# Performance work log

Hardware: AMD Instinct MI355X
Metric: run time of the kernel (lower is better)

The kernel has to match this reference:

```python
import jax, jax.numpy as jnp
import numpy as np

N_NODES = 50000
N_EDGES = 800000
IN_C, HID_C, OUT_C = 512, 256, 128


def setup_inputs() -> dict:
    key = jax.random.key(0)
    k1, k2, k3, k4, k5, k6 = jax.random.split(key, 6)
    x = jax.random.normal(k1, (N_NODES, IN_C), dtype=jnp.float32)
    edge_index = jax.random.randint(k2, (2, N_EDGES), 0, N_NODES, dtype=jnp.int64)
    # Glorot-ish init for linear weights, zero bias (PyG GCNConv default)
    W1 = jax.random.normal(k3, (IN_C, HID_C), dtype=jnp.float32) / np.sqrt(IN_C)
    b1 = jnp.zeros((HID_C,), dtype=jnp.float32)
    W2 = jax.random.normal(k4, (HID_C, OUT_C), dtype=jnp.float32) / np.sqrt(HID_C)
    b2 = jnp.zeros((OUT_C,), dtype=jnp.float32)
    return {"x": x, "edge_index": edge_index, "W1": W1, "b1": b1, "W2": W2, "b2": b2}


def _gcn_layer(h, src, dst, norm, W, b, n_nodes):
    # h: [N, Fin] -> [N, Fout];  out_i = sum_{j->i} norm_e * (h W)_j + b
    h = h @ W
    msg = h[src] * norm[:, None]            # [E+N, Fout]
    out = jax.ops.segment_sum(msg, dst, num_segments=n_nodes)
    return out + b


def reference(x, edge_index, W1, b1, W2, b2):
    n = x.shape[0]
    loops = jnp.arange(n, dtype=edge_index.dtype)
    src = jnp.concatenate([edge_index[0], loops])  # add self-loops
    dst = jnp.concatenate([edge_index[1], loops])
    # symmetric normalization D^{-1/2} (A+I) D^{-1/2}
    deg = jax.ops.segment_sum(jnp.ones_like(src, dtype=x.dtype), dst, num_segments=n)
    dinv = jax.lax.rsqrt(jnp.maximum(deg, 1.0))
    norm = dinv[src] * dinv[dst]

    h = _gcn_layer(x, src, dst, norm, W1, b1, n)
    h = jax.nn.relu(h)
    # dropout: identity in eval mode (training=False)
    out = _gcn_layer(h, src, dst, norm, W2, b2, n)
    return out
```

## Files before the change

kernel.cpp:

```cpp
#include <hip/hip_runtime.h>
#include <hip/hip_bf16.h>

#define N_NODES 50000
#define N_EDGES 800000
#define IN_C 512
#define HID_C 256
#define OUT_C 128
#define SCAN_BLOCKS 49

typedef short bf16x8 __attribute__((ext_vector_type(8)));
typedef float f32x4 __attribute__((ext_vector_type(4)));
typedef float f32x2 __attribute__((ext_vector_type(2)));

__device__ __forceinline__ float bf2f(unsigned short u) {
    return __uint_as_float(((unsigned)u) << 16);
}
__device__ __forceinline__ unsigned short f2bf(float f) {
    __hip_bfloat16 h = __float2bfloat16(f);
    return *(unsigned short*)&h;
}
__device__ __forceinline__ void acc_fp8x4(int dw, float* a) {
    f32x2 lo = __builtin_amdgcn_cvt_pk_f32_fp8(dw, false);
    f32x2 hi = __builtin_amdgcn_cvt_pk_f32_fp8(dw, true);
    a[0] += lo[0]; a[1] += lo[1]; a[2] += hi[0]; a[3] += hi[1];
}
__device__ __forceinline__ unsigned char f2fp8(float f) {
    return (unsigned char)(__builtin_amdgcn_cvt_pk_fp8_f32(f, 0.0f, 0, false) & 0xff);
}

__global__ void zero_counts_kernel(int* __restrict__ counts) {
    int i = blockIdx.x * blockDim.x + threadIdx.x;
    if (i < N_NODES) counts[i] = 0;
}

__global__ void count_kernel(const int* __restrict__ ei, int* __restrict__ counts) {
    int e = blockIdx.x * blockDim.x + threadIdx.x;
    if (e < N_EDGES) atomicAdd(&counts[ei[N_EDGES + e]], 1);
}

__global__ __launch_bounds__(256) void scan_part_kernel(const int* __restrict__ counts,
                                                        int* __restrict__ excl,
                                                        int* __restrict__ bsums) {
    __shared__ int tsum[256];
    const int t = threadIdx.x;
    const int base = blockIdx.x * 1024 + t * 4;
    int v[4];
    int s = 0;
#pragma unroll
    for (int j = 0; j < 4; j++) {
        int idx = base + j;
        v[j] = (idx < N_NODES) ? counts[idx] : 0;
        s += v[j];
    }
    tsum[t] = s;
    __syncthreads();
    for (int off = 1; off < 256; off <<= 1) {
        int add = (t >= off) ? tsum[t - off] : 0;
        __syncthreads();
        tsum[t] += add;
        __syncthreads();
    }
    int run = tsum[t] - s;
#pragma unroll
    for (int j = 0; j < 4; j++) {
        int idx = base + j;
        if (idx < N_NODES) excl[idx] = run;
        run += v[j];
    }
    if (t == 255) bsums[blockIdx.x] = tsum[255];
}

__global__ void scan_sums_kernel(int* __restrict__ bsums) {
    int ln = threadIdx.x;
    int v = (ln < SCAN_BLOCKS) ? bsums[ln] : 0;
    for (int off = 1; off < 64; off <<= 1) {
        int u = __shfl_up(v, off, 64);
        if (ln >= off) v += u;
    }
    int excl = __shfl_up(v, 1, 64);
    if (ln == 0) excl = 0;
    if (ln < SCAN_BLOCKS) bsums[ln] = excl;
}

__global__ void add_dinv_kernel(int* __restrict__ offsets, const int* __restrict__ bsums,
                                int* __restrict__ woff, const int* __restrict__ counts,
                                float* __restrict__ dinv) {
    int i = blockIdx.x * blockDim.x + threadIdx.x;
    if (i < N_NODES) {
        int o = offsets[i] + bsums[i >> 10];
        offsets[i] = o;
        woff[i] = o;
        dinv[i] = rsqrtf(1.0f + (float)counts[i]);
    }
    if (i == 0) offsets[N_NODES] = N_EDGES;
}

__global__ void fill_kernel(const int* __restrict__ ei, int* __restrict__ woff,
                            int* __restrict__ sedge) {
    int e = blockIdx.x * blockDim.x + threadIdx.x;
    if (e < N_EDGES) {
        int s = ei[e];
        int d = ei[N_EDGES + e];
        int pos = atomicAdd(&woff[d], 1);
        sedge[pos] = s;
    }
}

__global__ __launch_bounds__(256) void tcast_kernel(const float* __restrict__ W,
                                                    unsigned short* __restrict__ WT,
                                                    int K, int N) {
    int idx = blockIdx.x * 256 + threadIdx.x;
    int n = idx / K, k = idx - n * K;
    WT[idx] = f2bf(W[(size_t)k * N + n]);
}

__global__ __launch_bounds__(256) void gemm1_fused(const float* __restrict__ x,
                                                   const unsigned short* __restrict__ BT,
                                                   unsigned char* __restrict__ C,
                                                   const float* __restrict__ dinv) {
    __shared__ unsigned short As[64 * 32];
    __shared__ unsigned short Bs[256 * 32];

    const int tid = threadIdx.x;
    const int w = tid >> 6;
    const int ln = tid & 63;
    const int br = blockIdx.x * 64;

    const int quad = ln >> 4;
    const int l16 = ln & 15;
    const int wc = w * 64;

    const int ar = tid >> 2;
    const int ak = (tid & 3) * 8;

    int arow = br + ar;
    arow = arow < N_NODES ? arow : N_NODES - 1;
    const float* xrow = x + (size_t)arow * IN_C + ak;

    f32x4 acc[4][4];
#pragma unroll
    for (int mt = 0; mt < 4; mt++)
#pragma unroll
        for (int nt = 0; nt < 4; nt++) acc[mt][nt] = (f32x4){0.f, 0.f, 0.f, 0.f};

    for (int kk = 0; kk < IN_C; kk += 32) {
        float4 v0 = *(const float4*)(xrow + kk);
        float4 v1 = *(const float4*)(xrow + kk + 4);
        bf16x8 a8;
        a8[0] = (short)f2bf(v0.x); a8[1] = (short)f2bf(v0.y);
        a8[2] = (short)f2bf(v0.z); a8[3] = (short)f2bf(v0.w);
        a8[4] = (short)f2bf(v1.x); a8[5] = (short)f2bf(v1.y);
        a8[6] = (short)f2bf(v1.z); a8[7] = (short)f2bf(v1.w);
        *(bf16x8*)&As[ar * 32 + ak] = a8;
#pragma unroll
        for (int t = 0; t < 4; t++) {
            int n = (tid >> 2) + 64 * t;
            const unsigned short* gp = BT + (size_t)n * IN_C + kk + ak;
            unsigned short* lp = Bs + t * 2048 + tid * 8;
            __builtin_amdgcn_global_load_lds((const __attribute__((address_space(1))) void*)gp,
                                             (__attribute__((address_space(3))) void*)lp,
                                             16, 0, 0);
        }
        __syncthreads();

        bf16x8 af[4], bfr[4];
#pragma unroll
        for (int mt = 0; mt < 4; mt++)
            af[mt] = *(const bf16x8*)&As[(mt * 16 + l16) * 32 + quad * 8];
#pragma unroll
        for (int nt = 0; nt < 4; nt++)
            bfr[nt] = *(const bf16x8*)&Bs[(wc + nt * 16 + l16) * 32 + quad * 8];
#pragma unroll
        for (int mt = 0; mt < 4; mt++)
#pragma unroll
            for (int nt = 0; nt < 4; nt++)
                acc[mt][nt] = __builtin_amdgcn_mfma_f32_16x16x32_bf16(af[mt], bfr[nt],
                                                                      acc[mt][nt], 0, 0, 0);
        __syncthreads();
    }

#pragma unroll
    for (int mt = 0; mt < 4; mt++) {
#pragma unroll
        for (int r = 0; r < 4; r++) {
            int gr = br + mt * 16 + quad * 4 + r;
            if (gr < N_NODES) {
                float ds = dinv[gr];
#pragma unroll
                for (int nt = 0; nt < 4; nt++) {
                    int gc = wc + nt * 16 + l16;
                    C[(size_t)gr * HID_C + gc] = f2fp8(ds * acc[mt][nt][r]);
                }
            }
        }
    }
}

__global__ __launch_bounds__(256) void mfma_gemm_bt(const unsigned short* __restrict__ A,
                                                    const unsigned short* __restrict__ BT,
                                                    unsigned short* __restrict__ C,
                                                    const float* __restrict__ dinv,
                                                    int M, int N, int K) {
    __shared__ unsigned short As[128 * 32];
    __shared__ unsigned short Bs[128 * 32];

    const int tid = threadIdx.x;
    const int w = tid >> 6;
    const int ln = tid & 63;
    const int br = blockIdx.y * 128;
    const int bc = blockIdx.x * 128;

    const int quad = ln >> 4;
    const int l16 = ln & 15;
    const int wr = (w >> 1) * 64;
    const int wc = (w & 1) * 64;

    const int crow = ln >> 2;
    const int koff = (ln & 3) * 8;

    f32x4 acc[4][4];
#pragma unroll
    for (int mt = 0; mt < 4; mt++)
#pragma unroll
        for (int nt = 0; nt < 4; nt++) acc[mt][nt] = (f32x4){0.f, 0.f, 0.f, 0.f};

    for (int kk = 0; kk < K; kk += 32) {
#pragma unroll
        for (int t = 0; t < 2; t++) {
            int c = w + t * 4;
            int row = br + c * 16 + crow;
            row = row < M ? row : M - 1;
            const unsigned short* gp = A + (size_t)row * K + kk + koff;
            unsigned short* lp = As + c * 512 + ln * 8;
            __builtin_amdgcn_global_load_lds((const __attribute__((address_space(1))) void*)gp,
                                             (__attribute__((address_space(3))) void*)lp,
                                             16, 0, 0);
        }
#pragma unroll
        for (int t = 0; t < 2; t++) {
            int c = w + t * 4;
            int row = bc + c * 16 + crow;
            const unsigned short* gp = BT + (size_t)row * K + kk + koff;
            unsigned short* lp = Bs + c * 512 + ln * 8;
            __builtin_amdgcn_global_load_lds((const __attribute__((address_space(1))) void*)gp,
                                             (__attribute__((address_space(3))) void*)lp,
                                             16, 0, 0);
        }
        __syncthreads();

        bf16x8 af[4], bfr[4];
#pragma unroll
        for (int mt = 0; mt < 4; mt++)
            af[mt] = *(const bf16x8*)&As[(wr + mt * 16 + l16) * 32 + quad * 8];
#pragma unroll
        for (int nt = 0; nt < 4; nt++)
            bfr[nt] = *(const bf16x8*)&Bs[(wc + nt * 16 + l16) * 32 + quad * 8];
#pragma unroll
        for (int mt = 0; mt < 4; mt++)
#pragma unroll
            for (int nt = 0; nt < 4; nt++)
                acc[mt][nt] = __builtin_amdgcn_mfma_f32_16x16x32_bf16(af[mt], bfr[nt],
                                                                      acc[mt][nt], 0, 0, 0);
        __syncthreads();
    }

#pragma unroll
    for (int mt = 0; mt < 4; mt++) {
#pragma unroll
        for (int r = 0; r < 4; r++) {
            int gr = br + wr + mt * 16 + quad * 4 + r;
            if (gr < M) {
                float ds = dinv[gr];
#pragma unroll
                for (int nt = 0; nt < 4; nt++) {
                    int gc = bc + wc + nt * 16 + l16;
                    C[(size_t)gr * N + gc] = f2bf(ds * acc[mt][nt][r]);
                }
            }
        }
    }
}

__global__ __launch_bounds__(256) void gather1_fp8(const int* __restrict__ offsets,
                                                   const int* __restrict__ sedge,
                                                   const unsigned char* __restrict__ H,
                                                   const float* __restrict__ dinv,
                                                   const float* __restrict__ bias,
                                                   unsigned short* __restrict__ out) {
    const int node = blockIdx.x * 4 + (threadIdx.x >> 6);
    if (node >= N_NODES) return;
    const int ln = threadIdx.x & 63;
    const int g = ln >> 5;
    const int l = ln & 31;
    const int c0 = l * 8;

    float acc[8] = {};
    if (g == 0) {
        uint2 d = *(const uint2*)&H[(size_t)node * HID_C + c0];
        acc_fp8x4((int)d.x, acc);
        acc_fp8x4((int)d.y, acc + 4);
    }

    int k = offsets[node] + g;
    const int k1 = offsets[node + 1];
    for (; k + 6 < k1; k += 8) {
        int s0 = sedge[k], s1 = sedge[k + 2], s2 = sedge[k + 4], s3 = sedge[k + 6];
        uint2 d0 = *(const uint2*)&H[(size_t)s0 * HID_C + c0];
        uint2 d1 = *(const uint2*)&H[(size_t)s1 * HID_C + c0];
        uint2 d2 = *(const uint2*)&H[(size_t)s2 * HID_C + c0];
        uint2 d3 = *(const uint2*)&H[(size_t)s3 * HID_C + c0];
        acc_fp8x4((int)d0.x, acc); acc_fp8x4((int)d0.y, acc + 4);
        acc_fp8x4((int)d1.x, acc); acc_fp8x4((int)d1.y, acc + 4);
        acc_fp8x4((int)d2.x, acc); acc_fp8x4((int)d2.y, acc + 4);
        acc_fp8x4((int)d3.x, acc); acc_fp8x4((int)d3.y, acc + 4);
    }
    for (; k < k1; k += 2) {
        int s0 = sedge[k];
        uint2 d0 = *(const uint2*)&H[(size_t)s0 * HID_C + c0];
        acc_fp8x4((int)d0.x, acc);
        acc_fp8x4((int)d0.y, acc + 4);
    }

#pragma unroll
    for (int j = 0; j < 8; j++) acc[j] += __shfl_xor(acc[j], 32, 64);

    if (g == 0) {
        const float di = dinv[node];
        bf16x8 o;
#pragma unroll
        for (int j = 0; j < 8; j++)
            o[j] = (short)f2bf(fmaxf(di * acc[j] + bias[c0 + j], 0.0f));
        *(bf16x8*)&out[(size_t)node * HID_C + c0] = o;
    }
}

__global__ __launch_bounds__(256) void gather2_bf16(const int* __restrict__ offsets,
                                                    const int* __restrict__ sedge,
                                                    const unsigned short* __restrict__ H,
                                                    const float* __restrict__ dinv,
                                                    const float* __restrict__ bias,
                                                    float* __restrict__ out) {
    const int node = blockIdx.x * 4 + (threadIdx.x >> 6);
    if (node >= N_NODES) return;
    const int ln = threadIdx.x & 63;
    const int g = ln >> 4;
    const int l = ln & 15;
    const int c0 = l * 8;

    float acc[8] = {};
    if (g == 0) {
        bf16x8 h = *(const bf16x8*)&H[(size_t)node * OUT_C + c0];
#pragma unroll
        for (int j = 0; j < 8; j++) acc[j] = bf2f((unsigned short)h[j]);
    }

    int k = offsets[node] + g;
    const int k1 = offsets[node + 1];
    for (; k + 12 < k1; k += 16) {
        int s0 = sedge[k], s1 = sedge[k + 4], s2 = sedge[k + 8], s3 = sedge[k + 12];
        bf16x8 h0 = *(const bf16x8*)&H[(size_t)s0 * OUT_C + c0];
        bf16x8 h1 = *(const bf16x8*)&H[(size_t)s1 * OUT_C + c0];
        bf16x8 h2 = *(const bf16x8*)&H[(size_t)s2 * OUT_C + c0];
        bf16x8 h3 = *(const bf16x8*)&H[(size_t)s3 * OUT_C + c0];
#pragma unroll
        for (int j = 0; j < 8; j++) {
            acc[j] += bf2f((unsigned short)h0[j]);
            acc[j] += bf2f((unsigned short)h1[j]);
            acc[j] += bf2f((unsigned short)h2[j]);
            acc[j] += bf2f((unsigned short)h3[j]);
        }
    }
    for (; k < k1; k += 4) {
        int s0 = sedge[k];
        bf16x8 h0 = *(const bf16x8*)&H[(size_t)s0 * OUT_C + c0];
#pragma unroll
        for (int j = 0; j < 8; j++) acc[j] += bf2f((unsigned short)h0[j]);
    }

#pragma unroll
    for (int m = 16; m < 64; m <<= 1) {
#pragma unroll
        for (int j = 0; j < 8; j++) acc[j] += __shfl_xor(acc[j], m, 64);
    }

    if (g == 0) {
        const float di = dinv[node];
        float o[8];
#pragma unroll
        for (int j = 0; j < 8; j++) o[j] = di * acc[j] + bias[c0 + j];
        *(float4*)&out[(size_t)node * OUT_C + c0] = make_float4(o[0], o[1], o[2], o[3]);
        *(float4*)&out[(size_t)node * OUT_C + c0 + 4] = make_float4(o[4], o[5], o[6], o[7]);
    }
}

extern "C" void kernel_launch(void* const* d_in, const int* in_sizes, int n_in,
                              void* d_out, int out_size, void* d_ws, size_t ws_size,
                              hipStream_t stream) {
    const float* x  = (const float*)d_in[0];
    const int*   ei = (const int*)d_in[1];
    const float* W1 = (const float*)d_in[2];
    const float* b1 = (const float*)d_in[3];
    const float* W2 = (const float*)d_in[4];
    const float* b2 = (const float*)d_in[5];
    float* out = (float*)d_out;

    int*   counts     = (int*)d_ws;
    int*   offsets    = counts + 50048;
    int*   woff       = offsets + 50052;
    int*   bsums      = woff + 50048;
    float* dinv       = (float*)(bsums + 64);
    int*   sedge      = (int*)(dinv + 50048);
    unsigned short* W1T = (unsigned short*)(sedge + 800000);
    unsigned short* W2T = W1T + 131072;
    unsigned short* xb  = W2T + 32768;
    unsigned char*  H1  = (unsigned char*)(xb + (size_t)N_NODES * IN_C);
    unsigned short* A1b = xb;
    unsigned short* H2  = xb + (size_t)N_NODES * HID_C;

    zero_counts_kernel<<<(N_NODES + 255) / 256, 256, 0, stream>>>(counts);
    count_kernel<<<(N_EDGES + 255) / 256, 256, 0, stream>>>(ei, counts);
    scan_part_kernel<<<SCAN_BLOCKS, 256, 0, stream>>>(counts, offsets, bsums);
    scan_sums_kernel<<<1, 64, 0, stream>>>(bsums);
    add_dinv_kernel<<<(N_NODES + 255) / 256, 256, 0, stream>>>(offsets, bsums, woff, counts, dinv);
    fill_kernel<<<(N_EDGES + 255) / 256, 256, 0, stream>>>(ei, woff, sedge);

    tcast_kernel<<<(IN_C * HID_C) / 256, 256, 0, stream>>>(W1, W1T, IN_C, HID_C);
    tcast_kernel<<<(HID_C * OUT_C) / 256, 256, 0, stream>>>(W2, W2T, HID_C, OUT_C);

    gemm1_fused<<<(N_NODES + 63) / 64, 256, 0, stream>>>(x, W1T, H1, dinv);
    gather1_fp8<<<(N_NODES + 3) / 4, 256, 0, stream>>>(offsets, sedge, H1, dinv, b1, A1b);

    {
        dim3 grid(OUT_C / 128, (N_NODES + 127) / 128);
        mfma_gemm_bt<<<grid, 256, 0, stream>>>(A1b, W2T, H2, dinv, N_NODES, OUT_C, HID_C);
    }
    gather2_bf16<<<(N_NODES + 3) / 4, 256, 0, stream>>>(offsets, sedge, H2, dinv, b2, out);
}
```

Baseline: 386.2 us.

## Double-buffer LDS tiles in both GEMMs and shrink GEMM2 row tile

Both GEMM kernels now use two LDS buffers, so the global loads for the next K slice are issued before the MFMAs on the current slice and one barrier per iteration is removed. GEMM1 also delays the fp32-to-bf16 conversion of the next A tile until after the MFMAs. GEMM2 is specialised to fixed sizes with 64-row blocks instead of 128, which launches more blocks over the 50k rows. The cost is doubled LDS per block and more live registers, which may lower occupancy.

```diff
diff --git a/kernel.cpp b/kernel.cpp
--- a/kernel.cpp
+++ b/kernel.cpp
@@ -26,6 +26,10 @@
 }
 __device__ __forceinline__ unsigned char f2fp8(float f) {
     return (unsigned char)(__builtin_amdgcn_cvt_pk_fp8_f32(f, 0.0f, 0, false) & 0xff);
+}
+__device__ __forceinline__ void glds16(const void* gp, void* lp) {
+    __builtin_amdgcn_global_load_lds((const __attribute__((address_space(1))) void*)gp,
+                                     (__attribute__((address_space(3))) void*)lp, 16, 0, 0);
 }
 
 __global__ void zero_counts_kernel(int* __restrict__ counts) {
@@ -118,8 +122,8 @@
                                                    const unsigned short* __restrict__ BT,
                                                    unsigned char* __restrict__ C,
                                                    const float* __restrict__ dinv) {
-    __shared__ unsigned short As[64 * 32];
-    __shared__ unsigned short Bs[256 * 32];
+    __shared__ unsigned short As[2][64 * 32];
+    __shared__ unsigned short Bs[2][256 * 32];
 
     const int tid = threadIdx.x;
     const int w = tid >> 6;
@@ -136,6 +140,7 @@
     int arow = br + ar;
     arow = arow < N_NODES ? arow : N_NODES - 1;
     const float* xrow = x + (size_t)arow * IN_C + ak;
+    const int brow = (tid >> 2);
 
     f32x4 acc[4][4];
 #pragma unroll
@@ -143,39 +148,60 @@
 #pragma unroll
         for (int nt = 0; nt < 4; nt++) acc[mt][nt] = (f32x4){0.f, 0.f, 0.f, 0.f};
 
-    for (int kk = 0; kk < IN_C; kk += 32) {
-        float4 v0 = *(const float4*)(xrow + kk);
-        float4 v1 = *(const float4*)(xrow + kk + 4);
+    {
+        float4 v0 = *(const float4*)(xrow);
+        float4 v1 = *(const float4*)(xrow + 4);
+#pragma unroll
+        for (int tt = 0; tt < 4; tt++) {
+            const unsigned short* gp = BT + (size_t)(brow + 64 * tt) * IN_C + ak;
+            glds16(gp, &Bs[0][tt * 2048 + tid * 8]);
+        }
         bf16x8 a8;
         a8[0] = (short)f2bf(v0.x); a8[1] = (short)f2bf(v0.y);
         a8[2] = (short)f2bf(v0.z); a8[3] = (short)f2bf(v0.w);
         a8[4] = (short)f2bf(v1.x); a8[5] = (short)f2bf(v1.y);
         a8[6] = (short)f2bf(v1.z); a8[7] = (short)f2bf(v1.w);
-        *(bf16x8*)&As[ar * 32 + ak] = a8;
-#pragma unroll
-        for (int t = 0; t < 4; t++) {
-            int n = (tid >> 2) + 64 * t;
-            const unsigned short* gp = BT + (size_t)n * IN_C + kk + ak;
-            unsigned short* lp = Bs + t * 2048 + tid * 8;
-            __builtin_amdgcn_global_load_lds((const __attribute__((address_space(1))) void*)gp,
-                                             (__attribute__((address_space(3))) void*)lp,
-                                             16, 0, 0);
-        }
-        __syncthreads();
+        *(bf16x8*)&As[0][ar * 32 + ak] = a8;
+    }
+    __syncthreads();
+
+    for (int t = 0; t < 16; t++) {
+        const int buf = t & 1;
+        const int nxt = buf ^ 1;
+        const bool more = t < 15;
+        float4 v0, v1;
+        if (more) {
+            const int kk = (t + 1) * 32;
+            v0 = *(const float4*)(xrow + kk);
+            v1 = *(const float4*)(xrow + kk + 4);
+#pragma unroll
+            for (int tt = 0; tt < 4; tt++) {
+                const unsigned short* gp = BT + (size_t)(brow + 64 * tt) * IN_C + kk + ak;
+                glds16(gp, &Bs[nxt][tt * 2048 + tid * 8]);
+            }
+        }
 
         bf16x8 af[4], bfr[4];
 #pragma unroll
         for (int mt = 0; mt < 4; mt++)
-            af[mt] = *(const bf16x8*)&As[(mt * 16 + l16) * 32 + quad * 8];
+            af[mt] = *(const bf16x8*)&As[buf][(mt * 16 + l16) * 32 + quad * 8];
 #pragma unroll
         for (int nt = 0; nt < 4; nt++)
-            bfr[nt] = *(const bf16x8*)&Bs[(wc + nt * 16 + l16) * 32 + quad * 8];
+            bfr[nt] = *(const bf16x8*)&Bs[buf][(wc + nt * 16 + l16) * 32 + quad * 8];
 #pragma unroll
         for (int mt = 0; mt < 4; mt++)
 #pragma unroll
             for (int nt = 0; nt < 4; nt++)
                 acc[mt][nt] = __builtin_amdgcn_mfma_f32_16x16x32_bf16(af[mt], bfr[nt],
                                                                       acc[mt][nt], 0, 0, 0);
+        if (more) {
+            bf16x8 a8;
+            a8[0] = (short)f2bf(v0.x); a8[1] = (short)f2bf(v0.y);
+            a8[2] = (short)f2bf(v0.z); a8[3] = (short)f2bf(v0.w);
+            a8[4] = (short)f2bf(v1.x); a8[5] = (short)f2bf(v1.y);
+            a8[6] = (short)f2bf(v1.z); a8[7] = (short)f2bf(v1.w);
+            *(bf16x8*)&As[nxt][ar * 32 + ak] = a8;
+        }
         __syncthreads();
     }
 
@@ -196,67 +222,66 @@
     }
 }
 
-__global__ __launch_bounds__(256) void mfma_gemm_bt(const unsigned short* __restrict__ A,
-                                                    const unsigned short* __restrict__ BT,
-                                                    unsigned short* __restrict__ C,
-                                                    const float* __restrict__ dinv,
-                                                    int M, int N, int K) {
-    __shared__ unsigned short As[128 * 32];
-    __shared__ unsigned short Bs[128 * 32];
+__global__ __launch_bounds__(256) void gemm2_db(const unsigned short* __restrict__ A,
+                                                const unsigned short* __restrict__ BT,
+                                                unsigned short* __restrict__ C,
+                                                const float* __restrict__ dinv) {
+    __shared__ unsigned short As[2][64 * 32];
+    __shared__ unsigned short Bs[2][128 * 32];
 
     const int tid = threadIdx.x;
     const int w = tid >> 6;
     const int ln = tid & 63;
-    const int br = blockIdx.y * 128;
-    const int bc = blockIdx.x * 128;
+    const int br = blockIdx.x * 64;
 
     const int quad = ln >> 4;
     const int l16 = ln & 15;
-    const int wr = (w >> 1) * 64;
+    const int wr = (w >> 1) * 32;
     const int wc = (w & 1) * 64;
 
-    const int crow = ln >> 2;
-    const int koff = (ln & 3) * 8;
-
-    f32x4 acc[4][4];
-#pragma unroll
-    for (int mt = 0; mt < 4; mt++)
+    const int ak = (tid & 3) * 8;
+    const int trow = tid >> 2;
+
+    int arow = br + trow;
+    arow = arow < N_NODES ? arow : N_NODES - 1;
+    const unsigned short* agp0 = A + (size_t)arow * HID_C + ak;
+
+    f32x4 acc[2][4];
+#pragma unroll
+    for (int mt = 0; mt < 2; mt++)
 #pragma unroll
         for (int nt = 0; nt < 4; nt++) acc[mt][nt] = (f32x4){0.f, 0.f, 0.f, 0.f};
 
-    for (int kk = 0; kk < K; kk += 32) {
-#pragma unroll
-        for (int t = 0; t < 2; t++) {
-            int c = w + t * 4;
-            int row = br + c * 16 + crow;
-            row = row < M ? row : M - 1;
-            const unsigned short* gp = A + (size_t)row * K + kk + koff;
-            unsigned short* lp = As + c * 512 + ln * 8;
-            __builtin_amdgcn_global_load_lds((const __attribute__((address_space(1))) void*)gp,
-                                             (__attribute__((address_space(3))) void*)lp,
-                                             16, 0, 0);
-        }
-#pragma unroll
-        for (int t = 0; t < 2; t++) {
-            int c = w + t * 4;
-            int row = bc + c * 16 + crow;
-            const unsigned short* gp = BT + (size_t)row * K + kk + koff;
-            unsigned short* lp = Bs + c * 512 + ln * 8;
-            __builtin_amdgcn_global_load_lds((const __attribute__((address_space(1))) void*)gp,
-                                             (__attribute__((address_space(3))) void*)lp,
-                                             16, 0, 0);
-        }
-        __syncthreads();
-
-        bf16x8 af[4], bfr[4];
-#pragma unroll
-        for (int mt = 0; mt < 4; mt++)
-            af[mt] = *(const bf16x8*)&As[(wr + mt * 16 + l16) * 32 + quad * 8];
+    glds16(agp0, &As[0][tid * 8]);
+#pragma unroll
+    for (int tt = 0; tt < 2; tt++) {
+        const unsigned short* gp = BT + (size_t)(trow + 64 * tt) * HID_C + ak;
+        glds16(gp, &Bs[0][tt * 2048 + tid * 8]);
+    }
+    __syncthreads();
+
+    for (int t = 0; t < 8; t++) {
+        const int buf = t & 1;
+        const int nxt = buf ^ 1;
+        if (t < 7) {
+            const int kk = (t + 1) * 32;
+            glds16(agp0 + kk, &As[nxt][tid * 8]);
+#pragma unroll
+            for (int tt = 0; tt < 2; tt++) {
+                const unsigned short* gp = BT + (size_t)(trow + 64 * tt) * HID_C + kk + ak;
+                glds16(gp, &Bs[nxt][tt * 2048 + tid * 8]);
+            }
+        }
+
+        bf16x8 af[2], bfr[4];
+#pragma unroll
+        for (int mt = 0; mt < 2; mt++)
+            af[mt] = *(const bf16x8*)&As[buf][(wr + mt * 16 + l16) * 32 + quad * 8];
 #pragma unroll
         for (int nt = 0; nt < 4; nt++)
-            bfr[nt] = *(const bf16x8*)&Bs[(wc + nt * 16 + l16) * 32 + quad * 8];
-#pragma unroll
-        for (int mt = 0; mt < 4; mt++)
+            bfr[nt] = *(const bf16x8*)&Bs[buf][(wc + nt * 16 + l16) * 32 + quad * 8];
+#pragma unroll
+        for (int mt = 0; mt < 2; mt++)
 #pragma unroll
             for (int nt = 0; nt < 4; nt++)
                 acc[mt][nt] = __builtin_amdgcn_mfma_f32_16x16x32_bf16(af[mt], bfr[nt],
@@ -265,16 +290,16 @@
     }
 
 #pragma unroll
-    for (int mt = 0; mt < 4; mt++) {
+    for (int mt = 0; mt < 2; mt++) {
 #pragma unroll
         for (int r = 0; r < 4; r++) {
             int gr = br + wr + mt * 16 + quad * 4 + r;
-            if (gr < M) {
+            if (gr < N_NODES) {
                 float ds = dinv[gr];
 #pragma unroll
                 for (int nt = 0; nt < 4; nt++) {
-                    int gc = bc + wc + nt * 16 + l16;
-                    C[(size_t)gr * N + gc] = f2bf(ds * acc[mt][nt][r]);
+                    int gc = wc + nt * 16 + l16;
+                    C[(size_t)gr * OUT_C + gc] = f2bf(ds * acc[mt][nt][r]);
                 }
             }
         }
@@ -430,9 +455,6 @@
     gemm1_fused<<<(N_NODES + 63) / 64, 256, 0, stream>>>(x, W1T, H1, dinv);
     gather1_fp8<<<(N_NODES + 3) / 4, 256, 0, stream>>>(offsets, sedge, H1, dinv, b1, A1b);
 
-    {
-        dim3 grid(OUT_C / 128, (N_NODES + 127) / 128);
-        mfma_gemm_bt<<<grid, 256, 0, stream>>>(A1b, W2T, H2, dinv, N_NODES, OUT_C, HID_C);
-    }
+    gemm2_db<<<(N_NODES + 63) / 64, 256, 0, stream>>>(A1b, W2T, H2, dinv);
     gather2_bf16<<<(N_NODES + 3) / 4, 256, 0, stream>>>(offsets, sedge, H2, dinv, b2, out);
 }
```

Result: no change. 383.3 us (-0.7%).
